# Kernel optimization log

Measured on AMD Instinct MI355X. Metric: run time of the kernel, lower is better.

The kernel has to match this reference:

```python
import jax, jax.numpy as jnp
import numpy as np

HID = 1024   # utter_hidden * 2
UD = 512     # user_dim
B = 16384


def setup_inputs() -> dict:
    key = jax.random.key(0)
    ks = jax.random.split(key, 15)
    sx = 1.0 / np.sqrt(HID)
    sh = 1.0 / np.sqrt(UD)
    inp = {
        'encoder_hidden': jax.random.normal(ks[0], (B, HID), jnp.float32),
        'spk_vectors': jax.random.normal(ks[1], (B, UD), jnp.float32),
        'adr_vectors': jax.random.normal(ks[2], (B, UD), jnp.float32),
    }
    # torch Linear weights are [out, in]; bias=False everywhere
    names_x = ['WA_xr', 'WA_xp', 'WA_xz', 'WA_xh']
    names_h = ['WA_hr', 'WA_hp', 'WA_hz', 'WA_hh']
    names_v = ['VA_hr', 'VA_hp', 'VA_hz', 'VA_hh']
    i = 3
    for n in names_x:
        inp[n] = jax.random.uniform(ks[i], (UD, HID), jnp.float32, -sx, sx); i += 1
    for n in names_h + names_v:
        inp[n] = jax.random.uniform(ks[i], (UD, UD), jnp.float32, -sh, sh); i += 1
    return inp


def reference(encoder_hidden, spk_vectors, adr_vectors,
              WA_xr, WA_xp, WA_xz, WA_xh,
              WA_hr, WA_hp, WA_hz, WA_hh,
              VA_hr, VA_hp, VA_hz, VA_hh):
    def lin(x, W):  # torch nn.Linear (bias=False): x @ W.T
        return x @ W.T
    r_t = jax.nn.sigmoid(lin(encoder_hidden, WA_xr) + lin(spk_vectors, WA_hr) + lin(adr_vectors, VA_hr))
    p_t = jax.nn.sigmoid(lin(encoder_hidden, WA_xp) + lin(spk_vectors, WA_hp) + lin(adr_vectors, VA_hp))
    z_t = jax.nn.sigmoid(lin(encoder_hidden, WA_xz) + lin(spk_vectors, WA_hz) + lin(adr_vectors, VA_hz))
    h_tilde = jnp.tanh(lin(encoder_hidden, WA_xh) + lin(r_t * spk_vectors, WA_hh) + lin(p_t * adr_vectors, VA_hh))
    return (1.0 - z_t) * spk_vectors + z_t * h_tilde
```

## Files before the change

kernel.cpp:

```cpp
#include <hip/hip_runtime.h>
#include <hip/hip_bf16.h>
#include <stdint.h>


typedef short  short8  __attribute__((ext_vector_type(8)));
typedef unsigned short ushort8 __attribute__((ext_vector_type(8)));
typedef float  f32x4   __attribute__((ext_vector_type(4)));

static constexpr int Bn  = 16384;

__device__ __forceinline__ unsigned short f2bf(float x) {
  union { float f; unsigned u; } v; v.f = x;
  unsigned r = v.u + 0x7fffu + ((v.u >> 16) & 1u);
  return (unsigned short)(r >> 16);
}
__device__ __forceinline__ float bf2f(unsigned short h) {
  union { unsigned u; float f; } v; v.u = ((unsigned)h) << 16; return v.f;
}
__device__ __forceinline__ float sigm(float x) { return 1.0f / (1.0f + __expf(-x)); }
__device__ __forceinline__ float tanh_fast(float x) {
  return 2.0f / (1.0f + __expf(-2.0f * x)) - 1.0f;
}

__device__ __forceinline__ void gload_lds16(const void* g, void* l) {
  __builtin_amdgcn_global_load_lds((const __attribute__((address_space(1))) void*)g,
                                   (__attribute__((address_space(3))) void*)l,
                                   16, 0, 0);
}

__global__ __launch_bounds__(256) void pack_all(
    const float* __restrict__ X, const float* __restrict__ S, const float* __restrict__ A,
    const float* __restrict__ xr, const float* __restrict__ xp,
    const float* __restrict__ xz, const float* __restrict__ xh,
    const float* __restrict__ hr, const float* __restrict__ hp, const float* __restrict__ hz,
    const float* __restrict__ vr, const float* __restrict__ vp, const float* __restrict__ vz,
    unsigned short* __restrict__ U, unsigned short* __restrict__ W1)
{
  const int bid = blockIdx.x;
  const int tid = threadIdx.x;
  if (bid < 16384) {
    int idx = bid * 256 + tid;
    int b  = idx >> 8;
    int c8 = (idx & 255) << 3;
    const float* src = (c8 < 1024) ? X + (size_t)b * 1024 + c8
                     : (c8 < 1536) ? S + (size_t)b * 512 + (c8 - 1024)
                                   : A + (size_t)b * 512 + (c8 - 1536);
    f32x4 lo = *(const f32x4*)src;
    f32x4 hi = *(const f32x4*)(src + 4);
    ushort8 o;
    o[0] = f2bf(lo[0]); o[1] = f2bf(lo[1]); o[2] = f2bf(lo[2]); o[3] = f2bf(lo[3]);
    o[4] = f2bf(hi[0]); o[5] = f2bf(hi[1]); o[6] = f2bf(hi[2]); o[7] = f2bf(hi[3]);
    *(ushort8*)&U[(size_t)b * 2048 + c8] = o;
  } else {
    int idx = (bid - 16384) * 256 + tid;
    int n  = idx >> 8;
    int k8 = (idx & 255) << 3;
    int g = n >> 9, j = n & 511;
    const float* src = nullptr;
    if (k8 < 1024) {
      const float* x = (g == 0) ? xr : (g == 1) ? xp : (g == 2) ? xz : xh;
      src = x + (size_t)j * 1024 + k8;
    } else if (k8 < 1536) {
      if (g < 3) { const float* h = (g == 0) ? hr : (g == 1) ? hp : hz; src = h + (size_t)j * 512 + (k8 - 1024); }
    } else {
      if (g < 3) { const float* v = (g == 0) ? vr : (g == 1) ? vp : vz; src = v + (size_t)j * 512 + (k8 - 1536); }
    }
    ushort8 o;
    if (src) { for (int i = 0; i < 8; i++) o[i] = f2bf(src[i]); }
    else     { for (int i = 0; i < 8; i++) o[i] = 0; }
    *(ushort8*)&W1[(size_t)n * 2048 + k8] = o;
  }
}

__global__ __launch_bounds__(256) void pack_w2k(
    const float* __restrict__ hh, const float* __restrict__ vh,
    unsigned short* __restrict__ W2)
{
  int idx = blockIdx.x * 256 + threadIdx.x;
  int n  = idx >> 7;
  int k8 = (idx & 127) << 3;
  const float* src = (k8 < 512) ? hh + (size_t)n * 512 + k8
                                : vh + (size_t)n * 512 + (k8 - 512);
  ushort8 o;
  for (int i = 0; i < 8; i++) o[i] = f2bf(src[i]);
  *(ushort8*)&W2[(size_t)n * 1024 + k8] = o;
}

__global__ __launch_bounds__(256, 4) void gemm128_epi1(
    const unsigned short* __restrict__ Amat,
    const unsigned short* __restrict__ Bmat,
    const int K,
    unsigned short* __restrict__ U2, unsigned short* __restrict__ Zp,
    unsigned short* __restrict__ XHp)
{
  __shared__ __align__(16) char lds[32768];

  const int tid  = threadIdx.x;
  const int lane = tid & 63, wave = tid >> 6;
  const int wr = wave >> 1, wc = wave & 1;
  const int fr = lane & 15, fq = lane >> 4;

  const int k_xcd = blockIdx.x & 7;
  const int i_loc = (int)blockIdx.x >> 3;
  const int n0 = (i_loc & 15) * 128;
  const int m0 = (k_xcd * 16 + (i_loc >> 4)) * 128;

  const int Keff = (n0 >= 1536) ? 1024 : K;
  const int NT   = Keff >> 5;

  const int srow  = tid >> 2;
  const int sslot = (tid & 3) ^ ((srow >> 1) & 3);
  const unsigned short* gA = Amat + (size_t)(m0 + srow) * K + sslot * 8;
  const unsigned short* gB = Bmat + (size_t)(n0 + srow) * K + sslot * 8;
  const size_t K64r = (size_t)64 * K;

  const int swz  = (fq ^ ((fr >> 1) & 3)) << 4;
  const int aoff = (wr * 64 + fr) * 64 + swz;
  const int boff = 8192 + (wc * 64 + fr) * 64 + swz;

  f32x4 acc[4][4] = {};

  auto STAGE = [&](int buf, int tile) {
    const int bufo = buf << 14;
#pragma unroll
    for (int j = 0; j < 2; j++) {
      gload_lds16(gA + (size_t)j * K64r + (tile << 5), lds + bufo + j * 4096 + tid * 16);
      gload_lds16(gB + (size_t)j * K64r + (tile << 5), lds + bufo + 8192 + j * 4096 + tid * 16);
    }
  };
  auto COMPUTE = [&](int buf) {
    const int bufo = buf << 14;
    short8 b[4], a[4];
#pragma unroll
    for (int nt = 0; nt < 4; nt++)
      b[nt] = *(const short8*)(lds + bufo + boff + nt * 1024);
#pragma unroll
    for (int mt = 0; mt < 4; mt++)
      a[mt] = *(const short8*)(lds + bufo + aoff + mt * 1024);
#pragma unroll
    for (int mt = 0; mt < 4; mt++)
#pragma unroll
      for (int nt = 0; nt < 4; nt++)
        acc[mt][nt] = __builtin_amdgcn_mfma_f32_16x16x32_bf16(
            a[mt], b[nt], acc[mt][nt], 0, 0, 0);
  };

  STAGE(0, 0);
  __syncthreads();

  int cur = 0;
  for (int t = 0; t < NT - 1; ++t) {
    STAGE(cur ^ 1, t + 1);
    COMPUTE(cur);
    __syncthreads();
    cur ^= 1;
  }
  COMPUTE(cur);

#pragma unroll
  for (int mt = 0; mt < 4; mt++) {
#pragma unroll
    for (int nt = 0; nt < 4; nt++) {
      const int ncol = n0 + wc * 64 + nt * 16 + fr;
      const int gate = ncol >> 9, j = ncol & 511;
#pragma unroll
      for (int jj = 0; jj < 4; jj++) {
        const size_t rb = (size_t)(m0 + wr * 64 + mt * 16 + fq * 4 + jj);
        const float v = acc[mt][nt][jj];
        if (gate == 0) {
          const float s = bf2f(Amat[rb * 2048 + 1024 + j]);
          U2[rb * 1024 + j] = f2bf(sigm(v) * s);
        } else if (gate == 1) {
          const float a2 = bf2f(Amat[rb * 2048 + 1536 + j]);
          U2[rb * 1024 + 512 + j] = f2bf(sigm(v) * a2);
        } else if (gate == 2) {
          Zp[rb * 512 + j]  = f2bf(v);
        } else {
          XHp[rb * 512 + j] = f2bf(v);
        }
      }
    }
  }
}

__global__ __launch_bounds__(512, 1) void gemm2_fin(
    const unsigned short* __restrict__ U2,
    const unsigned short* __restrict__ W2,
    const unsigned short* __restrict__ Uu,
    const unsigned short* __restrict__ Zp,
    const unsigned short* __restrict__ XHp, float* __restrict__ Out)
{
  extern __shared__ char lds[];
  constexpr int K = 1024, NT = K >> 6;

  const int tid  = threadIdx.x;
  const int lane = tid & 63, wave = tid >> 6;
  const int wm = wave >> 1, wn = wave & 1;
  const int fr = lane & 15, fq = lane >> 4;

  const int k_xcd = blockIdx.x & 7;
  const int i_loc = (int)blockIdx.x >> 3;
  const int n0 = (i_loc & 3) * 128;
  const int m0 = (k_xcd * 8 + (i_loc >> 2)) * 256;

  const int srow  = tid >> 3;
  const int sslot = (tid & 7) ^ (srow & 7);
  const unsigned short* gA = U2 + (size_t)(m0 + srow) * K + sslot * 8;
  const unsigned short* gB = W2 + (size_t)(n0 + srow) * K + sslot * 8;
  const size_t K64 = (size_t)64 * K;

  int swz[2];
  swz[0] = ((fq    ) ^ (fr & 7)) << 4;
  swz[1] = ((fq + 4) ^ (fr & 7)) << 4;
  const int aoff = wm * 8192 + fr * 128;
  const int boff = 32768 + wn * 8192 + fr * 128;

  f32x4 acc[4][4] = {};

  auto STAGE = [&](int buf, int tile) {
    const int bufo = buf * 49152;
#pragma unroll
    for (int j = 0; j < 4; j++)
      gload_lds16(gA + (size_t)j * K64 + (tile << 6), lds + bufo + tid * 16 + j * 8192);
#pragma unroll
    for (int j = 0; j < 2; j++)
      gload_lds16(gB + (size_t)j * K64 + (tile << 6), lds + bufo + 32768 + tid * 16 + j * 8192);
  };
  auto COMPUTE = [&](int buf) {
    const int bufo = buf * 49152;
    short8 b[4][2];
#pragma unroll
    for (int ni = 0; ni < 4; ni++)
#pragma unroll
      for (int ks = 0; ks < 2; ks++)
        b[ni][ks] = *(const short8*)(lds + bufo + boff + ni * 2048 + swz[ks]);
#pragma unroll
    for (int c = 0; c < 2; c++) {
      short8 a[2][2];
#pragma unroll
      for (int i = 0; i < 2; i++)
#pragma unroll
        for (int ks = 0; ks < 2; ks++)
          a[i][ks] = *(const short8*)(lds + bufo + aoff + (c * 2 + i) * 2048 + swz[ks]);
#pragma unroll
      for (int i = 0; i < 2; i++)
#pragma unroll
        for (int ni = 0; ni < 4; ni++)
#pragma unroll
          for (int ks = 0; ks < 2; ks++)
            acc[c * 2 + i][ni] = __builtin_amdgcn_mfma_f32_16x16x32_bf16(
                a[i][ks], b[ni][ks], acc[c * 2 + i][ni], 0, 0, 0);
    }
  };

  STAGE(0, 0);
  __syncthreads();

  int cur = 0;
  for (int t = 0; t < NT - 1; ++t) {
    STAGE(cur ^ 1, t + 1);
    COMPUTE(cur);
    __syncthreads();
    cur ^= 1;
  }
  COMPUTE(cur);

#pragma unroll
  for (int mt = 0; mt < 4; mt++) {
#pragma unroll
    for (int nt = 0; nt < 4; nt++) {
      const int ncol = n0 + wn * 64 + nt * 16 + fr;
#pragma unroll
      for (int jj = 0; jj < 4; jj++) {
        const size_t rb = (size_t)(m0 + wm * 64 + mt * 16 + fq * 4 + jj);
        const size_t o = rb * 512 + ncol;
        const float z = sigm(bf2f(Zp[o]));
        const float h = tanh_fast(bf2f(XHp[o]) + acc[mt][nt][jj]);
        const float s = bf2f(Uu[rb * 2048 + 1024 + ncol]);
        Out[o] = (1.0f - z) * s + z * h;
      }
    }
  }
}


extern "C" void kernel_launch(void* const* d_in, const int* in_sizes, int n_in,
                              void* d_out, int out_size, void* d_ws, size_t ws_size,
                              hipStream_t stream) {
  const float* X   = (const float*)d_in[0];
  const float* S   = (const float*)d_in[1];
  const float* A   = (const float*)d_in[2];
  const float* Wxr = (const float*)d_in[3];
  const float* Wxp = (const float*)d_in[4];
  const float* Wxz = (const float*)d_in[5];
  const float* Wxh = (const float*)d_in[6];
  const float* Whr = (const float*)d_in[7];
  const float* Whp = (const float*)d_in[8];
  const float* Whz = (const float*)d_in[9];
  const float* Whh = (const float*)d_in[10];
  const float* Vhr = (const float*)d_in[11];
  const float* Vhp = (const float*)d_in[12];
  const float* Vhz = (const float*)d_in[13];
  const float* Vhh = (const float*)d_in[14];

  char* ws = (char*)d_ws;
  size_t off = 0;
  auto alloc = [&](size_t bytes) -> void* {
    void* p = ws + off;
    off += (bytes + 255) & ~(size_t)255;
    return p;
  };
  unsigned short* W1 = (unsigned short*)alloc((size_t)2048 * 2048 * 2);
  unsigned short* W2 = (unsigned short*)alloc((size_t)512 * 1024 * 2);
  unsigned short* U  = (unsigned short*)alloc((size_t)Bn * 2048 * 2);
  unsigned short* U2 = (unsigned short*)alloc((size_t)Bn * 1024 * 2);
  unsigned short* Zp = (unsigned short*)alloc((size_t)Bn * 512 * 2);
  unsigned short* XH = (unsigned short*)alloc((size_t)Bn * 512 * 2);

  pack_all<<<16384 + 2048, 256, 0, stream>>>(
      X, S, A, Wxr, Wxp, Wxz, Wxh, Whr, Whp, Whz, Vhr, Vhp, Vhz, U, W1);
  pack_w2k<<<256, 256, 0, stream>>>(Whh, Vhh, W2);

  (void)hipFuncSetAttribute((const void*)gemm2_fin,
                            hipFuncAttributeMaxDynamicSharedMemorySize, 98304);

  gemm128_epi1<<<2048, 256, 0, stream>>>(U, W1, 2048, U2, Zp, XH);

  gemm2_fin<<<256, 512, 98304, stream>>>(U2, W2, U, Zp, XH, (float*)d_out);
}
```

Measured before the change: 246.1 us.

## Retile second GEMM to 128x128 blocks with smaller K-tiles and static LDS

The second GEMM plus epilogue kernel moves from 256x128 tiles with 512 threads, a K-tile of 64 and 96KB of dynamic LDS to 128x128 tiles with 256 threads, a K-tile of 32 and 32KB of static LDS. The grid doubles to 512 blocks and launch bounds allow up to 4 blocks per CU. The aim is more blocks in flight on the 256-CU GPU and better latency hiding across blocks. In exchange, each block reuses less data per tile, runs twice as many K iterations with a sync each, and uses a new swizzle pattern.

Result: slower. 261.5 us (+6.2%).

```diff
diff --git a/kernel.cpp b/kernel.cpp
--- a/kernel.cpp
+++ b/kernel.cpp
@@ -183,74 +183,61 @@
   }
 }
 
-__global__ __launch_bounds__(512, 1) void gemm2_fin(
+__global__ __launch_bounds__(256, 4) void gemm2_fin128(
     const unsigned short* __restrict__ U2,
     const unsigned short* __restrict__ W2,
     const unsigned short* __restrict__ Uu,
     const unsigned short* __restrict__ Zp,
     const unsigned short* __restrict__ XHp, float* __restrict__ Out)
 {
-  extern __shared__ char lds[];
-  constexpr int K = 1024, NT = K >> 6;
+  __shared__ __align__(16) char lds[32768];
+  constexpr int K = 1024, NT = K >> 5;
 
   const int tid  = threadIdx.x;
   const int lane = tid & 63, wave = tid >> 6;
-  const int wm = wave >> 1, wn = wave & 1;
+  const int wr = wave >> 1, wc = wave & 1;
   const int fr = lane & 15, fq = lane >> 4;
 
   const int k_xcd = blockIdx.x & 7;
   const int i_loc = (int)blockIdx.x >> 3;
   const int n0 = (i_loc & 3) * 128;
-  const int m0 = (k_xcd * 8 + (i_loc >> 2)) * 256;
-
-  const int srow  = tid >> 3;
-  const int sslot = (tid & 7) ^ (srow & 7);
+  const int m0 = (k_xcd * 16 + (i_loc >> 2)) * 128;
+
+  const int srow  = tid >> 2;
+  const int sslot = (tid & 3) ^ ((srow >> 1) & 3);
   const unsigned short* gA = U2 + (size_t)(m0 + srow) * K + sslot * 8;
   const unsigned short* gB = W2 + (size_t)(n0 + srow) * K + sslot * 8;
-  const size_t K64 = (size_t)64 * K;
-
-  int swz[2];
-  swz[0] = ((fq    ) ^ (fr & 7)) << 4;
-  swz[1] = ((fq + 4) ^ (fr & 7)) << 4;
-  const int aoff = wm * 8192 + fr * 128;
-  const int boff = 32768 + wn * 8192 + fr * 128;
+  const size_t K64r = (size_t)64 * K;
+
+  const int swz  = (fq ^ ((fr >> 1) & 3)) << 4;
+  const int aoff = (wr * 64 + fr) * 64 + swz;
+  const int boff = 8192 + (wc * 64 + fr) * 64 + swz;
 
   f32x4 acc[4][4] = {};
 
   auto STAGE = [&](int buf, int tile) {
-    const int bufo = buf * 49152;
-#pragma unroll
-    for (int j = 0; j < 4; j++)
-      gload_lds16(gA + (size_t)j * K64 + (tile << 6), lds + bufo + tid * 16 + j * 8192);
-#pragma unroll
-    for (int j = 0; j < 2; j++)
-      gload_lds16(gB + (size_t)j * K64 + (tile << 6), lds + bufo + 32768 + tid * 16 + j * 8192);
+    const int bufo = buf << 14;
+#pragma unroll
+    for (int j = 0; j < 2; j++) {
+      gload_lds16(gA + (size_t)j * K64r + (tile << 5), lds + bufo + j * 4096 + tid * 16);
+      gload_lds16(gB + (size_t)j * K64r + (tile << 5), lds + bufo + 8192 + j * 4096 + tid * 16);
+    }
   };
   auto COMPUTE = [&](int buf) {
-    const int bufo = buf * 49152;
-    short8 b[4][2];
-#pragma unroll
-    for (int ni = 0; ni < 4; ni++)
-#pragma unroll
-      for (int ks = 0; ks < 2; ks++)
-        b[ni][ks] = *(const short8*)(lds + bufo + boff + ni * 2048 + swz[ks]);
-#pragma unroll
-    for (int c = 0; c < 2; c++) {
-      short8 a[2][2];
-#pragma unroll
-      for (int i = 0; i < 2; i++)
-#pragma unroll
-        for (int ks = 0; ks < 2; ks++)
-          a[i][ks] = *(const short8*)(lds + bufo + aoff + (c * 2 + i) * 2048 + swz[ks]);
-#pragma unroll
-      for (int i = 0; i < 2; i++)
-#pragma unroll
-        for (int ni = 0; ni < 4; ni++)
-#pragma unroll
-          for (int ks = 0; ks < 2; ks++)
-            acc[c * 2 + i][ni] = __builtin_amdgcn_mfma_f32_16x16x32_bf16(
-                a[i][ks], b[ni][ks], acc[c * 2 + i][ni], 0, 0, 0);
-    }
+    const int bufo = buf << 14;
+    short8 b[4], a[4];
+#pragma unroll
+    for (int nt = 0; nt < 4; nt++)
+      b[nt] = *(const short8*)(lds + bufo + boff + nt * 1024);
+#pragma unroll
+    for (int mt = 0; mt < 4; mt++)
+      a[mt] = *(const short8*)(lds + bufo + aoff + mt * 1024);
+#pragma unroll
+    for (int mt = 0; mt < 4; mt++)
+#pragma unroll
+      for (int nt = 0; nt < 4; nt++)
+        acc[mt][nt] = __builtin_amdgcn_mfma_f32_16x16x32_bf16(
+            a[mt], b[nt], acc[mt][nt], 0, 0, 0);
   };
 
   STAGE(0, 0);
@@ -269,10 +256,10 @@
   for (int mt = 0; mt < 4; mt++) {
 #pragma unroll
     for (int nt = 0; nt < 4; nt++) {
-      const int ncol = n0 + wn * 64 + nt * 16 + fr;
+      const int ncol = n0 + wc * 64 + nt * 16 + fr;
 #pragma unroll
       for (int jj = 0; jj < 4; jj++) {
-        const size_t rb = (size_t)(m0 + wm * 64 + mt * 16 + fq * 4 + jj);
+        const size_t rb = (size_t)(m0 + wr * 64 + mt * 16 + fq * 4 + jj);
         const size_t o = rb * 512 + ncol;
         const float z = sigm(bf2f(Zp[o]));
         const float h = tanh_fast(bf2f(XHp[o]) + acc[mt][nt][jj]);
@@ -321,10 +308,7 @@
       X, S, A, Wxr, Wxp, Wxz, Wxh, Whr, Whp, Whz, Vhr, Vhp, Vhz, U, W1);
   pack_w2k<<<256, 256, 0, stream>>>(Whh, Vhh, W2);
 
-  (void)hipFuncSetAttribute((const void*)gemm2_fin,
-                            hipFuncAttributeMaxDynamicSharedMemorySize, 98304);
-
   gemm128_epi1<<<2048, 256, 0, stream>>>(U, W1, 2048, U2, Zp, XH);
 
-  gemm2_fin<<<256, 512, 98304, stream>>>(U2, W2, U, Zp, XH, (float*)d_out);
-}
+  gemm2_fin128<<<512, 256, 0, stream>>>(U2, W2, U, Zp, XH, (float*)d_out);
+}
```
